# Optimization experiments

Hardware: AMD Instinct MI355X
Metric: run time of the kernel (lower is better)

Reference implementation:

```python
import jax, jax.numpy as jnp
import numpy as np

DIM = 256
NUM_HEADS = 8
REGIONS = [4, 4, 8, 8, 16, 16, 32, 32]  # per-head local window sizes
B, H_IMG, W_IMG = 8, 64, 64


def setup_inputs() -> dict:
    key = jax.random.key(0)
    ks = jax.random.split(key, 6)
    C = DIM
    s = 0.02
    return {
        'x': jax.random.normal(ks[0], (B, H_IMG * W_IMG, C), jnp.float32),
        'Wq': jax.random.normal(ks[1], (C, C), jnp.float32) * s,
        'Wkv': jax.random.normal(ks[2], (C, 2 * C), jnp.float32) * s,
        'Wlkv': jax.random.normal(ks[3], (C, 2 * C), jnp.float32) * s,
        'Wproj': jax.random.normal(ks[4], (C, C), jnp.float32) * s,
        'bproj': jnp.zeros((C,), jnp.float32),
        'H': H_IMG,
        'W': W_IMG,
    }


def _attn(q, k, v, scale):
    # softmax(q k^T * scale) v, batched over leading dims
    a = jax.nn.softmax(jnp.einsum('...qd,...kd->...qk', q, k) * scale, axis=-1)
    return jnp.einsum('...qk,...kd->...qd', a, v)


def reference(x, Wq, Wkv, Wlkv, Wproj, bproj, H, W):
    Bn, N, C = x.shape
    nh = NUM_HEADS
    Ch = C // nh
    scale = Ch ** -0.5
    M = max(REGIONS)

    q = (x @ Wq).reshape(Bn, N, nh, Ch).transpose(0, 2, 1, 3)            # [B,nh,N,Ch]
    kv = (x @ Wkv).reshape(Bn, N, 2, nh, Ch).transpose(2, 0, 3, 1, 4)    # [2,B,nh,N,Ch]
    k, v = kv[0], kv[1]

    head_outs, global_q = [], []
    for i, p in enumerate(REGIONS):
        def patch(a, p=p):  # [B,N,Ch] -> [B,NP,p*p,Ch]
            a = a.reshape(Bn, H // p, p, W // p, p, Ch)
            return a.transpose(0, 1, 3, 2, 4, 5).reshape(Bn, -1, p * p, Ch)
        qp, kp, vp = patch(q[:, i]), patch(k[:, i]), patch(v[:, i])
        # global query: mean over patches -> [B,p,p,Ch], bilinear upsample to [M,M]
        qg = qp.mean(axis=1).reshape(Bn, p, p, Ch)
        if M // p > 1:
            qg = jax.image.resize(qg, (Bn, M, M, Ch), method='bilinear')
        global_q.append(qg.reshape(Bn, M * M, Ch))
        out = _attn(qp, kp, vp, scale)                                    # [B,NP,p*p,Ch]
        head_outs.append(out.reshape(Bn, N, Ch))  # flatten in PATCH order (matches torch code)

    attn_fused = jnp.stack(head_outs, axis=1).transpose(0, 2, 1, 3).reshape(Bn, N, C)
    Q_g = jnp.stack(global_q, axis=1).transpose(0, 2, 1, 3).reshape(Bn, M * M, C)

    # blend: adaptive avg-pool attn_fused to [M,M] (exact pooling since M|H), cross-attend, upsample
    kh, kw = H // M, W // M
    pooled = attn_fused.reshape(Bn, M, kh, M, kw, C).mean(axis=(2, 4)).reshape(Bn, M * M, C)
    kv2 = (pooled @ Wlkv).reshape(Bn, M * M, 2, nh, Ch).transpose(2, 0, 3, 1, 4)
    k2, v2 = kv2[0], kv2[1]
    Qr = Q_g.reshape(Bn, M * M, nh, Ch).transpose(0, 2, 1, 3)             # [B,nh,M^2,Ch]
    gl = _attn(Qr, k2, v2, scale)                                          # [B,nh,M^2,Ch]
    gl = gl.transpose(0, 2, 1, 3).reshape(Bn, M, M, C)
    gl = jax.image.resize(gl, (Bn, H, W, C), method='bilinear').reshape(Bn, N, C)

    return (attn_fused + gl) @ Wproj + bproj
```

## Files before the change

### kernel.cpp

```cpp
#include <hip/hip_runtime.h>
#include <math.h>


typedef __attribute__((ext_vector_type(8))) short bf16x8;
typedef __attribute__((ext_vector_type(4))) short bf16x4;
typedef __attribute__((ext_vector_type(4))) float f32x4;

__device__ inline float bf2f(unsigned short u) {
  union { unsigned int i; float f; } v; v.i = ((unsigned int)u) << 16; return v.f;
}
__device__ inline unsigned short f2bf(float x) {
  union { float f; unsigned int i; } v; v.f = x;
  return (unsigned short)((v.i + 0x7FFFu + ((v.i >> 16) & 1u)) >> 16);
}
__device__ inline unsigned cvtpk(float lo, float hi) {
  unsigned r;
  asm("v_cvt_pk_bf16_f32 %0, %1, %2" : "=v"(r) : "v"(lo), "v"(hi));
  return r;
}

#define CEXP_SCALE 0.25503485947f

__global__ __launch_bounds__(256) void msa_xcast_r17(
    const float* __restrict__ x, unsigned short* __restrict__ xb)
{
  const size_t i = ((size_t)blockIdx.x * 256 + threadIdx.x) * 8;
  const float4 v0 = *reinterpret_cast<const float4*>(&x[i]);
  const float4 v1 = *reinterpret_cast<const float4*>(&x[i + 4]);
  bf16x8 o;
  o[0] = (short)f2bf(v0.x); o[1] = (short)f2bf(v0.y);
  o[2] = (short)f2bf(v0.z); o[3] = (short)f2bf(v0.w);
  o[4] = (short)f2bf(v1.x); o[5] = (short)f2bf(v1.y);
  o[6] = (short)f2bf(v1.z); o[7] = (short)f2bf(v1.w);
  *reinterpret_cast<bf16x8*>(&xb[i]) = o;
}

__global__ __launch_bounds__(256) void msa_wcast_r17(
    const float* __restrict__ Wq, const float* __restrict__ Wkv,
    const float* __restrict__ Wlkv, const float* __restrict__ Wproj,
    unsigned short* __restrict__ Wqkvt, unsigned short* __restrict__ Wlkvt,
    unsigned short* __restrict__ Wprjt)
{
  const int id = blockIdx.x * 256 + threadIdx.x;
  if (id < 196608) {
    const int r = id >> 8, k = id & 255;
    const float v = (r < 256) ? Wq[(size_t)k * 256 + r] : Wkv[(size_t)k * 512 + (r - 256)];
    Wqkvt[id] = f2bf(v);
  } else if (id < 327680) {
    const int j = id - 196608;
    const int n = j >> 8, k = j & 255;
    Wlkvt[j] = f2bf(Wlkv[(size_t)k * 512 + n]);
  } else if (id < 393216) {
    const int j = id - 327680;
    const int n = j >> 8, k = j & 255;
    Wprjt[j] = f2bf(Wproj[(size_t)k * 256 + n]);
  }
}

__global__ __launch_bounds__(256) void msa_gemm_mfma_r17(
    const unsigned short* __restrict__ Ab, const unsigned short* __restrict__ Wt,
    const float* __restrict__ bias, float* __restrict__ Cf,
    unsigned short* __restrict__ Cb, int K, int N, int qcols)
{
  __shared__ __align__(16) unsigned short A_lds[128][40];
  __shared__ __align__(16) unsigned short B_lds[128][40];

  const int tid = threadIdx.x;
  const int wave = tid >> 6, lane = tid & 63;
  const int l15 = lane & 15, g = lane >> 4;

  const int gx = gridDim.x;
  const int nwg = gx * gridDim.y;
  const int lin = blockIdx.y * gx + blockIdx.x;
  const int qq = nwg >> 3;
  const int virt = (lin & 7) * qq + (lin >> 3);
  const int by = virt / gx, bx = virt - by * gx;
  const int bm = by * 128, bn = bx * 128;

  const int wr = (wave >> 1) * 64, wc = (wave & 1) * 64;

  f32x4 acc[4][4] = {};

  for (int k0 = 0; k0 < K; k0 += 32) {
    __syncthreads();
#pragma unroll
    for (int s = 0; s < 2; ++s) {
      const int id = tid + s * 256;
      const int row = id >> 2, sg = (id & 3) << 3;
      *reinterpret_cast<bf16x8*>(&A_lds[row][sg]) =
          *reinterpret_cast<const bf16x8*>(&Ab[(size_t)(bm + row) * K + k0 + sg]);
      *reinterpret_cast<bf16x8*>(&B_lds[row][sg]) =
          *reinterpret_cast<const bf16x8*>(&Wt[(size_t)(bn + row) * K + k0 + sg]);
    }
    __syncthreads();

    bf16x8 a_frag[4], b_frag[4];
#pragma unroll
    for (int mi = 0; mi < 4; ++mi)
      a_frag[mi] = *reinterpret_cast<const bf16x8*>(&A_lds[wr + mi * 16 + l15][g << 3]);
#pragma unroll
    for (int ni = 0; ni < 4; ++ni)
      b_frag[ni] = *reinterpret_cast<const bf16x8*>(&B_lds[wc + ni * 16 + l15][g << 3]);
#pragma unroll
    for (int mi = 0; mi < 4; ++mi)
#pragma unroll
      for (int ni = 0; ni < 4; ++ni)
        acc[mi][ni] = __builtin_amdgcn_mfma_f32_16x16x32_bf16(
            a_frag[mi], b_frag[ni], acc[mi][ni], 0, 0, 0);
  }

#pragma unroll
  for (int mi = 0; mi < 4; ++mi)
#pragma unroll
    for (int ni = 0; ni < 4; ++ni) {
      const int col = bn + wc + ni * 16 + l15;
      const float cs = (col < qcols) ? CEXP_SCALE : 1.0f;
#pragma unroll
      for (int i = 0; i < 4; ++i) {
        const int row = bm + wr + mi * 16 + g * 4 + i;
        float v = acc[mi][ni][i];
        if (bias) v += bias[col];
        v *= cs;
        const size_t idx = (size_t)row * N + col;
        if (Cb) Cb[idx] = f2bf(v); else Cf[idx] = v;
      }
    }
}

__device__ inline void tile_step_r17(
    const bf16x8 k0, const bf16x8 k1, const bf16x8 v0, const bf16x8 v1,
    const bf16x8 ones, const bf16x8 qf, f32x4& o0, f32x4& o1, f32x4& o2)
{
  const f32x4 zc = {0.f, 0.f, 0.f, 0.f};
  const f32x4 st0 = __builtin_amdgcn_mfma_f32_16x16x32_bf16(k0, qf, zc, 0, 0, 0);
  const f32x4 st1 = __builtin_amdgcn_mfma_f32_16x16x32_bf16(k1, qf, zc, 0, 0, 0);
  const float e00 = exp2f(st0[0]);
  const float e01 = exp2f(st0[1]);
  const float e02 = exp2f(st0[2]);
  const float e03 = exp2f(st0[3]);
  const float e10 = exp2f(st1[0]);
  const float e11 = exp2f(st1[1]);
  const float e12 = exp2f(st1[2]);
  const float e13 = exp2f(st1[3]);
  const unsigned u0 = cvtpk(e00, e01);
  const unsigned u1 = cvtpk(e02, e03);
  const unsigned u2 = cvtpk(e10, e11);
  const unsigned u3 = cvtpk(e12, e13);
  uint4 pu = make_uint4(u0, u1, u2, u3);
  const bf16x8 pb = *reinterpret_cast<const bf16x8*>(&pu);
  o2 = __builtin_amdgcn_mfma_f32_16x16x32_bf16(ones, pb, o2, 0, 0, 0);
  o0 = __builtin_amdgcn_mfma_f32_16x16x32_bf16(v0, pb, o0, 0, 0, 0);
  o1 = __builtin_amdgcn_mfma_f32_16x16x32_bf16(v1, pb, o1, 0, 0, 0);
}

__global__ __launch_bounds__(256) void msa_attn_local_r17(
    const unsigned short* __restrict__ xqkv, unsigned short* __restrict__ attnb)
{
  __shared__ __align__(16) unsigned short K_lds[64][40];
  __shared__ __align__(16) unsigned short V_lds[32][68];

  const int fx = blockIdx.x;
  const int b = blockIdx.y;
  const int tid = threadIdx.x;

  bf16x8 ones;
#pragma unroll
  for (int i = 0; i < 8; ++i) ones[i] = (short)0x3F80;

  if (fx < 32) {
    const int head = fx >> 4;
    const int nq = (fx & 15) * 256 + tid;
    const int patch = nq >> 4;
    const int t = nq & 15;
    const int hb = patch >> 4, wb = patch & 15;
    const int n = (hb * 4 + (t >> 2)) * 64 + (wb * 4 + (t & 3));

    float qr[32];
    {
      const bf16x8* q8 = reinterpret_cast<const bf16x8*>(
          xqkv + ((size_t)b * 4096 + n) * 768 + head * 32);
#pragma unroll
      for (int i = 0; i < 4; ++i) {
        const bf16x8 v = q8[i];
#pragma unroll
        for (int j = 0; j < 8; ++j) qr[i * 8 + j] = bf2f((unsigned short)v[j]);
      }
    }
    float l = 0.f;
    float acc[32] = {};
    const int kbase = (hb * 4) * 64 + wb * 4;
    for (int kk = 0; kk < 16; ++kk) {
      const int nk = kbase + (kk >> 2) * 64 + (kk & 3);
      const unsigned short* rowp = xqkv + ((size_t)b * 4096 + nk) * 768 + head * 32;
      const bf16x8* k8p = reinterpret_cast<const bf16x8*>(rowp + 256);
      const bf16x8* v8p = reinterpret_cast<const bf16x8*>(rowp + 512);
      float s = 0.f;
#pragma unroll
      for (int i = 0; i < 4; ++i) {
        const bf16x8 k8 = k8p[i];
#pragma unroll
        for (int j = 0; j < 8; ++j) s = fmaf(qr[i * 8 + j], bf2f((unsigned short)k8[j]), s);
      }
      const float p = exp2f(s);
      l += p;
#pragma unroll
      for (int i = 0; i < 4; ++i) {
        const bf16x8 v8 = v8p[i];
#pragma unroll
        for (int j = 0; j < 8; ++j)
          acc[i * 8 + j] = fmaf(p, bf2f((unsigned short)v8[j]), acc[i * 8 + j]);
      }
    }
    const float inv = 1.f / l;
    unsigned short* dst = attnb + ((size_t)b * 4096 + nq) * 256 + head * 32;
#pragma unroll
    for (int c = 0; c < 32; ++c) dst[c] = f2bf(acc[c] * inv);
    return;
  }

  const int wave = tid >> 6, lane = tid & 63;
  const int q16 = lane & 15, h = lane >> 4;
  const int skey = tid >> 2;
  const int sh = tid & 3;

  if (fx < 160) {
    const int j = fx - 32;
    const int head = 2 + (j >> 6);
    const int patch = j & 63;
    const int hb = patch >> 3, wb = patch & 7;
    const int base = (hb * 8) * 64 + wb * 8;
    const int nq = patch * 64 + wave * 16 + q16;
    const int t = nq & 63;
    const int n = base + ((t >> 3) << 6) + (t & 7);

    const bf16x8 qfrag = *reinterpret_cast<const bf16x8*>(
        xqkv + ((size_t)b * 4096 + n) * 768 + head * 32 + 8 * h);

    f32x4 o0 = {0.f,0.f,0.f,0.f}, o1 = {0.f,0.f,0.f,0.f}, o2 = {0.f,0.f,0.f,0.f};
    {
      const int nk = base + ((skey >> 3) << 6) + (skey & 7);
      const unsigned short* row = xqkv + ((size_t)b * 4096 + nk) * 768 + head * 32;
      *reinterpret_cast<bf16x8*>(&K_lds[skey][8 * sh]) =
          *reinterpret_cast<const bf16x8*>(row + 256 + 8 * sh);
      const bf16x8 v = *reinterpret_cast<const bf16x8*>(row + 512 + 8 * sh);
#pragma unroll
      for (int jj = 0; jj < 8; ++jj)
        V_lds[8 * sh + jj][skey] = (unsigned short)v[jj];
    }
    __syncthreads();

#pragma unroll
    for (int sub = 0; sub < 2; ++sub) {
      const int s32 = sub * 32;
      const bf16x8 k0 = *reinterpret_cast<const bf16x8*>(&K_lds[s32 + q16][8 * h]);
      const bf16x8 k1 = *reinterpret_cast<const bf16x8*>(&K_lds[s32 + 16 + q16][8 * h]);
      const bf16x4 va0 = *reinterpret_cast<const bf16x4*>(&V_lds[q16][s32 + 4 * h]);
      const bf16x4 vb0 = *reinterpret_cast<const bf16x4*>(&V_lds[q16][s32 + 16 + 4 * h]);
      const bf16x4 va1 = *reinterpret_cast<const bf16x4*>(&V_lds[16 + q16][s32 + 4 * h]);
      const bf16x4 vb1 = *reinterpret_cast<const bf16x4*>(&V_lds[16 + q16][s32 + 16 + 4 * h]);
      bf16x8 v0, v1;
#pragma unroll
      for (int i = 0; i < 4; ++i) {
        v0[i] = va0[i]; v0[4 + i] = vb0[i];
        v1[i] = va1[i]; v1[4 + i] = vb1[i];
      }
      tile_step_r17(k0, k1, v0, v1, ones, qfrag, o0, o1, o2);
    }

    const float inv = 1.f / o2[0];
    unsigned short* dst = attnb + ((size_t)b * 4096 + nq) * 256 + head * 32;
    uint2 w0, w1;
    w0.x = (unsigned)f2bf(o0[0] * inv) | ((unsigned)f2bf(o0[1] * inv) << 16);
    w0.y = (unsigned)f2bf(o0[2] * inv) | ((unsigned)f2bf(o0[3] * inv) << 16);
    w1.x = (unsigned)f2bf(o1[0] * inv) | ((unsigned)f2bf(o1[1] * inv) << 16);
    w1.y = (unsigned)f2bf(o1[2] * inv) | ((unsigned)f2bf(o1[3] * inv) << 16);
    *reinterpret_cast<uint2*>(dst + 4 * h) = w0;
    *reinterpret_cast<uint2*>(dst + 16 + 4 * h) = w1;
    return;
  }

  {
    const int j = fx - 160;
    const int head = 4 + (j >> 4);
    const int xb = j & 15;
    const int lp = (head < 6) ? 4 : 5;
    const int p = 1 << lp;
    const int pm1 = p - 1;
    const int P2 = p * p;
    const int patch = (xb * 256) >> (2 * lp);
    const int nbp = 64 >> lp;
    const int hb = patch / nbp, wb = patch - (patch / nbp) * nbp;
    const int base = ((hb << lp)) * 64 + (wb << lp);

    const int q0 = xb * 256 + wave * 64;
    const int nqA = q0 + q16, nqB = q0 + 16 + q16, nqC = q0 + 32 + q16, nqD = q0 + 48 + q16;

    bf16x8 qfA, qfB, qfC, qfD;
    {
      int tt = nqA & (P2 - 1);
      qfA = *reinterpret_cast<const bf16x8*>(
          xqkv + ((size_t)b * 4096 + base + ((tt >> lp) << 6) + (tt & pm1)) * 768 + head * 32 + 8 * h);
      tt = nqB & (P2 - 1);
      qfB = *reinterpret_cast<const bf16x8*>(
          xqkv + ((size_t)b * 4096 + base + ((tt >> lp) << 6) + (tt & pm1)) * 768 + head * 32 + 8 * h);
      tt = nqC & (P2 - 1);
      qfC = *reinterpret_cast<const bf16x8*>(
          xqkv + ((size_t)b * 4096 + base + ((tt >> lp) << 6) + (tt & pm1)) * 768 + head * 32 + 8 * h);
      tt = nqD & (P2 - 1);
      qfD = *reinterpret_cast<const bf16x8*>(
          xqkv + ((size_t)b * 4096 + base + ((tt >> lp) << 6) + (tt & pm1)) * 768 + head * 32 + 8 * h);
    }

    f32x4 o0A = {0.f,0.f,0.f,0.f}, o1A = {0.f,0.f,0.f,0.f}, o2A = {0.f,0.f,0.f,0.f};
    f32x4 o0B = {0.f,0.f,0.f,0.f}, o1B = {0.f,0.f,0.f,0.f}, o2B = {0.f,0.f,0.f,0.f};
    f32x4 o0C = {0.f,0.f,0.f,0.f}, o1C = {0.f,0.f,0.f,0.f}, o2C = {0.f,0.f,0.f,0.f};
    f32x4 o0D = {0.f,0.f,0.f,0.f}, o1D = {0.f,0.f,0.f,0.f}, o2D = {0.f,0.f,0.f,0.f};

    {
      const int nk0 = base + ((skey >> lp) << 6) + (skey & pm1);
      const unsigned short* row = xqkv + ((size_t)b * 4096 + nk0) * 768 + head * 32;
      const bf16x8 kr = *reinterpret_cast<const bf16x8*>(row + 256 + 8 * sh);
      const bf16x8 vr = *reinterpret_cast<const bf16x8*>(row + 512 + 8 * sh);
      *reinterpret_cast<bf16x8*>(&K_lds[skey][8 * sh]) = kr;
#pragma unroll
      for (int jj = 0; jj < 8; ++jj)
        V_lds[8 * sh + jj][skey] = (unsigned short)vr[jj];
    }
    __syncthreads();

    for (int kc = 0; kc < P2; kc += 64) {
      const bool more = (kc + 64) < P2;
      bf16x8 krn = {}, vrn = {};
      if (more) {
        const int kk = kc + 64 + skey;
        const int nk = base + ((kk >> lp) << 6) + (kk & pm1);
        const unsigned short* row = xqkv + ((size_t)b * 4096 + nk) * 768 + head * 32;
        krn = *reinterpret_cast<const bf16x8*>(row + 256 + 8 * sh);
        vrn = *reinterpret_cast<const bf16x8*>(row + 512 + 8 * sh);
      }

#pragma unroll
      for (int sub = 0; sub < 2; ++sub) {
        const int s32 = sub * 32;
        const bf16x8 k0 = *reinterpret_cast<const bf16x8*>(&K_lds[s32 + q16][8 * h]);
        const bf16x8 k1 = *reinterpret_cast<const bf16x8*>(&K_lds[s32 + 16 + q16][8 * h]);
        const bf16x4 va0 = *reinterpret_cast<const bf16x4*>(&V_lds[q16][s32 + 4 * h]);
        const bf16x4 vb0 = *reinterpret_cast<const bf16x4*>(&V_lds[q16][s32 + 16 + 4 * h]);
        const bf16x4 va1 = *reinterpret_cast<const bf16x4*>(&V_lds[16 + q16][s32 + 4 * h]);
        const bf16x4 vb1 = *reinterpret_cast<const bf16x4*>(&V_lds[16 + q16][s32 + 16 + 4 * h]);
        bf16x8 v0, v1;
#pragma unroll
        for (int i = 0; i < 4; ++i) {
          v0[i] = va0[i]; v0[4 + i] = vb0[i];
          v1[i] = va1[i]; v1[4 + i] = vb1[i];
        }
        tile_step_r17(k0, k1, v0, v1, ones, qfA, o0A, o1A, o2A);
        tile_step_r17(k0, k1, v0, v1, ones, qfB, o0B, o1B, o2B);
        tile_step_r17(k0, k1, v0, v1, ones, qfC, o0C, o1C, o2C);
        tile_step_r17(k0, k1, v0, v1, ones, qfD, o0D, o1D, o2D);
      }
      __syncthreads();
      if (more) {
        *reinterpret_cast<bf16x8*>(&K_lds[skey][8 * sh]) = krn;
#pragma unroll
        for (int jj = 0; jj < 8; ++jj)
          V_lds[8 * sh + jj][skey] = (unsigned short)vrn[jj];
      }
      __syncthreads();
    }

#define R17L_EPI(O0, O1, O2, NQ)                                               \
    {                                                                          \
      const float inv = 1.f / O2[0];                                           \
      unsigned short* dst = attnb + ((size_t)b * 4096 + (NQ)) * 256 + head * 32;\
      uint2 w0, w1;                                                            \
      w0.x = (unsigned)f2bf(O0[0] * inv) | ((unsigned)f2bf(O0[1] * inv) << 16);\
      w0.y = (unsigned)f2bf(O0[2] * inv) | ((unsigned)f2bf(O0[3] * inv) << 16);\
      w1.x = (unsigned)f2bf(O1[0] * inv) | ((unsigned)f2bf(O1[1] * inv) << 16);\
      w1.y = (unsigned)f2bf(O1[2] * inv) | ((unsigned)f2bf(O1[3] * inv) << 16);\
      *reinterpret_cast<uint2*>(dst + 4 * h) = w0;                             \
      *reinterpret_cast<uint2*>(dst + 16 + 4 * h) = w1;                        \
    }
    R17L_EPI(o0A, o1A, o2A, nqA)
    R17L_EPI(o0B, o1B, o2B, nqB)
    R17L_EPI(o0C, o1C, o2C, nqC)
    R17L_EPI(o0D, o1D, o2D, nqD)
#undef R17L_EPI
  }
}

__global__ __launch_bounds__(256) void msa_attn_glob_r17(
    const unsigned short* __restrict__ Qg, const unsigned short* __restrict__ kv2,
    float* __restrict__ gl)
{
  __shared__ __align__(16) unsigned short K_lds[64][40];
  __shared__ __align__(16) unsigned short V_lds[32][68];

  const int tid = threadIdx.x;
  const int wave = tid >> 6, lane = tid & 63;
  const int q16 = lane & 15, h = lane >> 4;
  const int b = blockIdx.y;
  const int head = blockIdx.z;

  bf16x8 ones;
#pragma unroll
  for (int i = 0; i < 8; ++i) ones[i] = (short)0x3F80;

  const int q0 = blockIdx.x * 256 + wave * 64;
  const int nqA = q0 + q16, nqB = q0 + 16 + q16, nqC = q0 + 32 + q16, nqD = q0 + 48 + q16;

  const bf16x8 qfA = *reinterpret_cast<const bf16x8*>(
      Qg + ((size_t)b * 1024 + nqA) * 256 + head * 32 + 8 * h);
  const bf16x8 qfB = *reinterpret_cast<const bf16x8*>(
      Qg + ((size_t)b * 1024 + nqB) * 256 + head * 32 + 8 * h);
  const bf16x8 qfC = *reinterpret_cast<const bf16x8*>(
      Qg + ((size_t)b * 1024 + nqC) * 256 + head * 32 + 8 * h);
  const bf16x8 qfD = *reinterpret_cast<const bf16x8*>(
      Qg + ((size_t)b * 1024 + nqD) * 256 + head * 32 + 8 * h);

  f32x4 o0A = {0.f,0.f,0.f,0.f}, o1A = {0.f,0.f,0.f,0.f}, o2A = {0.f,0.f,0.f,0.f};
  f32x4 o0B = {0.f,0.f,0.f,0.f}, o1B = {0.f,0.f,0.f,0.f}, o2B = {0.f,0.f,0.f,0.f};
  f32x4 o0C = {0.f,0.f,0.f,0.f}, o1C = {0.f,0.f,0.f,0.f}, o2C = {0.f,0.f,0.f,0.f};
  f32x4 o0D = {0.f,0.f,0.f,0.f}, o1D = {0.f,0.f,0.f,0.f}, o2D = {0.f,0.f,0.f,0.f};

  const int skey = tid >> 2;
  const int sh = tid & 3;

  {
    const unsigned short* row = kv2 + ((size_t)b * 1024 + skey) * 512 + head * 32;
    const bf16x8 kr = *reinterpret_cast<const bf16x8*>(row + 8 * sh);
    const bf16x8 vr = *reinterpret_cast<const bf16x8*>(row + 256 + 8 * sh);
    *reinterpret_cast<bf16x8*>(&K_lds[skey][8 * sh]) = kr;
#pragma unroll
    for (int jj = 0; jj < 8; ++jj)
      V_lds[8 * sh + jj][skey] = (unsigned short)vr[jj];
  }
  __syncthreads();

  for (int kc = 0; kc < 1024; kc += 64) {
    const bool more = (kc + 64) < 1024;
    bf16x8 krn = {}, vrn = {};
    if (more) {
      const unsigned short* row = kv2 + ((size_t)b * 1024 + kc + 64 + skey) * 512 + head * 32;
      krn = *reinterpret_cast<const bf16x8*>(row + 8 * sh);
      vrn = *reinterpret_cast<const bf16x8*>(row + 256 + 8 * sh);
    }

#pragma unroll
    for (int sub = 0; sub < 2; ++sub) {
      const int s32 = sub * 32;
      const bf16x8 k0 = *reinterpret_cast<const bf16x8*>(&K_lds[s32 + q16][8 * h]);
      const bf16x8 k1 = *reinterpret_cast<const bf16x8*>(&K_lds[s32 + 16 + q16][8 * h]);
      const bf16x4 va0 = *reinterpret_cast<const bf16x4*>(&V_lds[q16][s32 + 4 * h]);
      const bf16x4 vb0 = *reinterpret_cast<const bf16x4*>(&V_lds[q16][s32 + 16 + 4 * h]);
      const bf16x4 va1 = *reinterpret_cast<const bf16x4*>(&V_lds[16 + q16][s32 + 4 * h]);
      const bf16x4 vb1 = *reinterpret_cast<const bf16x4*>(&V_lds[16 + q16][s32 + 16 + 4 * h]);
      bf16x8 v0, v1;
#pragma unroll
      for (int i = 0; i < 4; ++i) {
        v0[i] = va0[i]; v0[4 + i] = vb0[i];
        v1[i] = va1[i]; v1[4 + i] = vb1[i];
      }
      tile_step_r17(k0, k1, v0, v1, ones, qfA, o0A, o1A, o2A);
      tile_step_r17(k0, k1, v0, v1, ones, qfB, o0B, o1B, o2B);
      tile_step_r17(k0, k1, v0, v1, ones, qfC, o0C, o1C, o2C);
      tile_step_r17(k0, k1, v0, v1, ones, qfD, o0D, o1D, o2D);
    }
    __syncthreads();
    if (more) {
      *reinterpret_cast<bf16x8*>(&K_lds[skey][8 * sh]) = krn;
#pragma unroll
      for (int jj = 0; jj < 8; ++jj)
        V_lds[8 * sh + jj][skey] = (unsigned short)vrn[jj];
    }
    __syncthreads();
  }

#define R17G_EPI(O0, O1, O2, NQ)                                               \
  {                                                                            \
    const float inv = 1.f / O2[0];                                             \
    float* dst = gl + ((size_t)b * 1024 + (NQ)) * 256 + head * 32;             \
    float4 w0, w1;                                                             \
    w0.x = O0[0] * inv; w0.y = O0[1] * inv;                                    \
    w0.z = O0[2] * inv; w0.w = O0[3] * inv;                                    \
    w1.x = O1[0] * inv; w1.y = O1[1] * inv;                                    \
    w1.z = O1[2] * inv; w1.w = O1[3] * inv;                                    \
    *reinterpret_cast<float4*>(dst + 4 * h) = w0;                              \
    *reinterpret_cast<float4*>(dst + 16 + 4 * h) = w1;                         \
  }
  R17G_EPI(o0A, o1A, o2A, nqA)
  R17G_EPI(o0B, o1B, o2B, nqB)
  R17G_EPI(o0C, o1C, o2C, nqC)
  R17G_EPI(o0D, o1D, o2D, nqD)
#undef R17G_EPI
}

__global__ __launch_bounds__(256) void msa_qg_reduce_r17(
    const unsigned short* __restrict__ xqkv, float* __restrict__ qg_all)
{
  __shared__ float red[256];
  const int head = blockIdx.z;
  const int lp = (head < 2) ? 2 : (head < 4) ? 3 : (head < 6) ? 4 : 5;
  const int p = 1 << lp;
  const int P2 = p * p;
  const int nbp = 64 >> lp;
  const int npat = nbp * nbp;
  const int R = (lp <= 3) ? 8 : 1;
  const int total = P2 * 32 * R;
  const int gid = blockIdx.x * 256 + threadIdx.x;
  if (gid >= total) return;
  const int b = blockIdx.y;

  const int c = gid & 31;
  const int tr = gid >> 5;
  const int r = tr & (R - 1);
  const int t = tr >> ((R == 8) ? 3 : 0);
  const int hp = t >> lp, wp = t & (p - 1);

  const unsigned short* src = xqkv + (size_t)b * 4096 * 768 + head * 32 + c;
  float s = 0.f;
  for (int j = r; j < npat; j += R) {
    const int hb = j / nbp, wb = j - (j / nbp) * nbp;
    const int n = ((hb << lp) + hp) * 64 + (wb << lp) + wp;
    s += bf2f(src[(size_t)n * 768]);
  }

  if (R == 8) {
    red[threadIdx.x] = s;
    __syncthreads();
    if (r < 4) red[threadIdx.x] += red[threadIdx.x + 128];
    __syncthreads();
    if (r < 2) red[threadIdx.x] += red[threadIdx.x + 64];
    __syncthreads();
    if (r == 0) {
      s = red[threadIdx.x] + red[threadIdx.x + 32];
      qg_all[((size_t)b * 8 + head) * 32768 + (size_t)t * 32 + c] = s / (float)npat;
    }
  } else {
    qg_all[((size_t)b * 8 + head) * 32768 + (size_t)t * 32 + c] = s / (float)npat;
  }
}

__global__ __launch_bounds__(256) void msa_qg_upsample_r17(
    const float* __restrict__ qg_all, unsigned short* __restrict__ Qg)
{
  const int head = blockIdx.z;
  const int p = (head < 2) ? 4 : (head < 4) ? 8 : (head < 6) ? 16 : 32;
  const int e = blockIdx.x * 256 + threadIdx.x;
  const int b = blockIdx.y;
  const int mlin = e >> 5, c = e & 31;
  const int mi = mlin >> 5, mj = mlin & 31;
  const float* src = qg_all + ((size_t)b * 8 + head) * 32768;
  float v;
  if (p == 32) {
    v = src[(size_t)mlin * 32 + c];
  } else {
    const float s = (float)p / 32.0f;
    const float xf = (mj + 0.5f) * s - 0.5f;
    const float yf = (mi + 0.5f) * s - 0.5f;
    const float xfl = floorf(xf), yfl = floorf(yf);
    const float fx = xf - xfl, fy = yf - yfl;
    const int x0 = (int)xfl, y0 = (int)yfl;
    const int x0c = max(0, min(p - 1, x0)), x1c = max(0, min(p - 1, x0 + 1));
    const int y0c = max(0, min(p - 1, y0)), y1c = max(0, min(p - 1, y0 + 1));
    const float v00 = src[(size_t)(y0c * p + x0c) * 32 + c];
    const float v01 = src[(size_t)(y0c * p + x1c) * 32 + c];
    const float v10 = src[(size_t)(y1c * p + x0c) * 32 + c];
    const float v11 = src[(size_t)(y1c * p + x1c) * 32 + c];
    v = (1.f - fy) * ((1.f - fx) * v00 + fx * v01)
      + fy * ((1.f - fx) * v10 + fx * v11);
  }
  Qg[((size_t)b * 1024 + mlin) * 256 + head * 32 + c] = f2bf(v);
}

__global__ __launch_bounds__(256) void msa_pool_r17(
    const unsigned short* __restrict__ attn, unsigned short* __restrict__ pooled)
{
  const int c = threadIdx.x;
  const int mlin = blockIdx.x;
  const int b = blockIdx.y;
  const int mi = mlin >> 5, mj = mlin & 31;
  const size_t base = (size_t)b * 4096;
  const int r0 = mi * 2, q0 = mj * 2;
  float s = bf2f(attn[(base + (r0 * 64 + q0)) * 256 + c])
          + bf2f(attn[(base + (r0 * 64 + q0 + 1)) * 256 + c])
          + bf2f(attn[(base + ((r0 + 1) * 64 + q0)) * 256 + c])
          + bf2f(attn[(base + ((r0 + 1) * 64 + q0 + 1)) * 256 + c]);
  pooled[((size_t)b * 1024 + mlin) * 256 + c] = f2bf(s * 0.25f);
}

__global__ __launch_bounds__(256) void msa_blend_r17(
    const float* __restrict__ gl, unsigned short* __restrict__ attn)
{
  const int c = threadIdx.x;
  const int n = blockIdx.x;
  const int b = blockIdx.y;
  const int hh = n >> 6, w = n & 63;
  const float xf = (w + 0.5f) * 0.5f - 0.5f;
  const float yf = (hh + 0.5f) * 0.5f - 0.5f;
  const float xfl = floorf(xf), yfl = floorf(yf);
  const float fx = xf - xfl, fy = yf - yfl;
  const int x0 = (int)xfl, y0 = (int)yfl;
  const int x0c = max(0, min(31, x0)), x1c = max(0, min(31, x0 + 1));
  const int y0c = max(0, min(31, y0)), y1c = max(0, min(31, y0 + 1));
  const float* g = gl + (size_t)b * 1024 * 256;
  const float v00 = g[(size_t)(y0c * 32 + x0c) * 256 + c];
  const float v01 = g[(size_t)(y0c * 32 + x1c) * 256 + c];
  const float v10 = g[(size_t)(y1c * 32 + x0c) * 256 + c];
  const float v11 = g[(size_t)(y1c * 32 + x1c) * 256 + c];
  const float v = (1.f - fy) * ((1.f - fx) * v00 + fx * v01)
                + fy * ((1.f - fx) * v10 + fx * v11);
  const size_t idx = ((size_t)b * 4096 + n) * 256 + c;
  attn[idx] = f2bf(bf2f(attn[idx]) + v);
}

extern "C" void kernel_launch(void* const* d_in, const int* in_sizes, int n_in,
                              void* d_out, int out_size, void* d_ws, size_t ws_size,
                              hipStream_t stream)
{
  const float* x     = (const float*)d_in[0];
  const float* Wq    = (const float*)d_in[1];
  const float* Wkv   = (const float*)d_in[2];
  const float* Wlkv  = (const float*)d_in[3];
  const float* Wproj = (const float*)d_in[4];
  const float* bproj = (const float*)d_in[5];

  char* ws = (char*)d_ws;
  unsigned short* xqkv  = (unsigned short*)(ws + 0);
  unsigned short* attnb = (unsigned short*)(ws + 50331648ull);
  unsigned short* Qg    = (unsigned short*)(ws + 67108864ull);
  float* qg_all = (float*)(ws + 71303168ull);
  unsigned short* Wqkvt = (unsigned short*)(ws + 79691776ull);
  unsigned short* Wlkvt = (unsigned short*)(ws + 80084992ull);
  unsigned short* Wprjt = (unsigned short*)(ws + 80347136ull);
  float* gl     = (float*)(ws + 80478208ull);
  unsigned short* xb    = (unsigned short*)(ws + 88866816ull);
  unsigned short* pooled = (unsigned short*)(ws + 0);
  unsigned short* kv2    = (unsigned short*)(ws + 16777216ull);

  msa_xcast_r17<<<dim3(4096), 256, 0, stream>>>(x, xb);
  msa_wcast_r17<<<dim3(1536), 256, 0, stream>>>(Wq, Wkv, Wlkv, Wproj, Wqkvt, Wlkvt, Wprjt);

  msa_gemm_mfma_r17<<<dim3(6, 256), 256, 0, stream>>>(xb, Wqkvt, nullptr, nullptr, xqkv, 256, 768, 256);

  msa_qg_reduce_r17<<<dim3(128, 8, 8), 256, 0, stream>>>(xqkv, qg_all);
  msa_qg_upsample_r17<<<dim3(128, 8, 8), 256, 0, stream>>>(qg_all, Qg);

  msa_attn_local_r17<<<dim3(224, 8), 256, 0, stream>>>(xqkv, attnb);

  msa_pool_r17<<<dim3(1024, 8), 256, 0, stream>>>(attnb, pooled);
  msa_gemm_mfma_r17<<<dim3(4, 64), 256, 0, stream>>>(pooled, Wlkvt, nullptr, nullptr, kv2, 256, 512, 0);

  msa_attn_glob_r17<<<dim3(4, 8, 8), 256, 0, stream>>>(Qg, kv2, gl);

  msa_blend_r17<<<dim3(4096, 8), 256, 0, stream>>>(gl, attnb);
  msa_gemm_mfma_r17<<<dim3(2, 256), 256, 0, stream>>>(attnb, Wprjt, bproj, (float*)d_out, nullptr, 256, 256, 0);

  (void)in_sizes; (void)n_in; (void)out_size; (void)ws_size;
}
```

Measured before the change: 218.6 us.

## Split long attention key ranges across two workgroups with combine kernels

```diff
diff --git a/kernel.cpp b/kernel.cpp
--- a/kernel.cpp
+++ b/kernel.cpp
@@ -21,7 +21,7 @@
 
 #define CEXP_SCALE 0.25503485947f
 
-__global__ __launch_bounds__(256) void msa_xcast_r17(
+__global__ __launch_bounds__(256) void msa_xcast_r18(
     const float* __restrict__ x, unsigned short* __restrict__ xb)
 {
   const size_t i = ((size_t)blockIdx.x * 256 + threadIdx.x) * 8;
@@ -35,7 +35,7 @@
   *reinterpret_cast<bf16x8*>(&xb[i]) = o;
 }
 
-__global__ __launch_bounds__(256) void msa_wcast_r17(
+__global__ __launch_bounds__(256) void msa_wcast_r18(
     const float* __restrict__ Wq, const float* __restrict__ Wkv,
     const float* __restrict__ Wlkv, const float* __restrict__ Wproj,
     unsigned short* __restrict__ Wqkvt, unsigned short* __restrict__ Wlkvt,
@@ -57,7 +57,7 @@
   }
 }
 
-__global__ __launch_bounds__(256) void msa_gemm_mfma_r17(
+__global__ __launch_bounds__(256) void msa_gemm_mfma_r18(
     const unsigned short* __restrict__ Ab, const unsigned short* __restrict__ Wt,
     const float* __restrict__ bias, float* __restrict__ Cf,
     unsigned short* __restrict__ Cb, int K, int N, int qcols)
@@ -127,7 +127,7 @@
     }
 }
 
-__device__ inline void tile_step_r17(
+__device__ inline void tile_step_r18(
     const bf16x8 k0, const bf16x8 k1, const bf16x8 v0, const bf16x8 v1,
     const bf16x8 ones, const bf16x8 qf, f32x4& o0, f32x4& o1, f32x4& o2)
 {
@@ -153,8 +153,9 @@
   o1 = __builtin_amdgcn_mfma_f32_16x16x32_bf16(v1, pb, o1, 0, 0, 0);
 }
 
-__global__ __launch_bounds__(256) void msa_attn_local_r17(
-    const unsigned short* __restrict__ xqkv, unsigned short* __restrict__ attnb)
+__global__ __launch_bounds__(256) void msa_attn_local_r18(
+    const unsigned short* __restrict__ xqkv, unsigned short* __restrict__ attnb,
+    float* __restrict__ po, float* __restrict__ pl)
 {
   __shared__ __align__(16) unsigned short K_lds[64][40];
   __shared__ __align__(16) unsigned short V_lds[32][68];
@@ -264,7 +265,7 @@
         v0[i] = va0[i]; v0[4 + i] = vb0[i];
         v1[i] = va1[i]; v1[4 + i] = vb1[i];
       }
-      tile_step_r17(k0, k1, v0, v1, ones, qfrag, o0, o1, o2);
+      tile_step_r18(k0, k1, v0, v1, ones, qfrag, o0, o1, o2);
     }
 
     const float inv = 1.f / o2[0];
@@ -279,97 +280,106 @@
     return;
   }
 
+  int head, lp, xb2, split, kstart, kend;
+  if (fx < 192) {
+    const int j = fx - 160;
+    head = 4 + (j >> 4); xb2 = j & 15; split = 0; lp = 4;
+    kstart = 0; kend = 256;
+  } else {
+    const int j = fx - 192;
+    head = 6 + (j >> 5);
+    const int r = j & 31;
+    xb2 = r >> 1; split = r & 1; lp = 5;
+    kstart = split * 512; kend = kstart + 512;
+  }
+  const int p = 1 << lp;
+  const int pm1 = p - 1;
+  const int P2 = p * p;
+  const int nbp = 64 >> lp;
+  const int patch = (xb2 * 256) >> (2 * lp);
+  const int hb = patch / nbp, wb = patch - (patch / nbp) * nbp;
+  const int base = ((hb << lp)) * 64 + (wb << lp);
+
+  const int q0 = xb2 * 256 + wave * 64;
+  const int nqA = q0 + q16, nqB = q0 + 16 + q16, nqC = q0 + 32 + q16, nqD = q0 + 48 + q16;
+
+  bf16x8 qfA, qfB, qfC, qfD;
   {
-    const int j = fx - 160;
-    const int head = 4 + (j >> 4);
-    const int xb = j & 15;
-    const int lp = (head < 6) ? 4 : 5;
-    const int p = 1 << lp;
-    const int pm1 = p - 1;
-    const int P2 = p * p;
-    const int patch = (xb * 256) >> (2 * lp);
-    const int nbp = 64 >> lp;
-    const int hb = patch / nbp, wb = patch - (patch / nbp) * nbp;
-    const int base = ((hb << lp)) * 64 + (wb << lp);
-
-    const int q0 = xb * 256 + wave * 64;
-    const int nqA = q0 + q16, nqB = q0 + 16 + q16, nqC = q0 + 32 + q16, nqD = q0 + 48 + q16;
-
-    bf16x8 qfA, qfB, qfC, qfD;
-    {
-      int tt = nqA & (P2 - 1);
-      qfA = *reinterpret_cast<const bf16x8*>(
-          xqkv + ((size_t)b * 4096 + base + ((tt >> lp) << 6) + (tt & pm1)) * 768 + head * 32 + 8 * h);
-      tt = nqB & (P2 - 1);
-      qfB = *reinterpret_cast<const bf16x8*>(
-          xqkv + ((size_t)b * 4096 + base + ((tt >> lp) << 6) + (tt & pm1)) * 768 + head * 32 + 8 * h);
-      tt = nqC & (P2 - 1);
-      qfC = *reinterpret_cast<const bf16x8*>(
-          xqkv + ((size_t)b * 4096 + base + ((tt >> lp) << 6) + (tt & pm1)) * 768 + head * 32 + 8 * h);
-      tt = nqD & (P2 - 1);
-      qfD = *reinterpret_cast<const bf16x8*>(
-          xqkv + ((size_t)b * 4096 + base + ((tt >> lp) << 6) + (tt & pm1)) * 768 + head * 32 + 8 * h);
-    }
-
-    f32x4 o0A = {0.f,0.f,0.f,0.f}, o1A = {0.f,0.f,0.f,0.f}, o2A = {0.f,0.f,0.f,0.f};
-    f32x4 o0B = {0.f,0.f,0.f,0.f}, o1B = {0.f,0.f,0.f,0.f}, o2B = {0.f,0.f,0.f,0.f};
-    f32x4 o0C = {0.f,0.f,0.f,0.f}, o1C = {0.f,0.f,0.f,0.f}, o2C = {0.f,0.f,0.f,0.f};
-    f32x4 o0D = {0.f,0.f,0.f,0.f}, o1D = {0.f,0.f,0.f,0.f}, o2D = {0.f,0.f,0.f,0.f};
-
-    {
-      const int nk0 = base + ((skey >> lp) << 6) + (skey & pm1);
-      const unsigned short* row = xqkv + ((size_t)b * 4096 + nk0) * 768 + head * 32;
-      const bf16x8 kr = *reinterpret_cast<const bf16x8*>(row + 256 + 8 * sh);
-      const bf16x8 vr = *reinterpret_cast<const bf16x8*>(row + 512 + 8 * sh);
-      *reinterpret_cast<bf16x8*>(&K_lds[skey][8 * sh]) = kr;
+    int tt = nqA & (P2 - 1);
+    qfA = *reinterpret_cast<const bf16x8*>(
+        xqkv + ((size_t)b * 4096 + base + ((tt >> lp) << 6) + (tt & pm1)) * 768 + head * 32 + 8 * h);
+    tt = nqB & (P2 - 1);
+    qfB = *reinterpret_cast<const bf16x8*>(
+        xqkv + ((size_t)b * 4096 + base + ((tt >> lp) << 6) + (tt & pm1)) * 768 + head * 32 + 8 * h);
+    tt = nqC & (P2 - 1);
+    qfC = *reinterpret_cast<const bf16x8*>(
+        xqkv + ((size_t)b * 4096 + base + ((tt >> lp) << 6) + (tt & pm1)) * 768 + head * 32 + 8 * h);
+    tt = nqD & (P2 - 1);
+    qfD = *reinterpret_cast<const bf16x8*>(
+        xqkv + ((size_t)b * 4096 + base + ((tt >> lp) << 6) + (tt & pm1)) * 768 + head * 32 + 8 * h);
+  }
+
+  f32x4 o0A = {0.f,0.f,0.f,0.f}, o1A = {0.f,0.f,0.f,0.f}, o2A = {0.f,0.f,0.f,0.f};
+  f32x4 o0B = {0.f,0.f,0.f,0.f}, o1B = {0.f,0.f,0.f,0.f}, o2B = {0.f,0.f,0.f,0.f};
+  f32x4 o0C = {0.f,0.f,0.f,0.f}, o1C = {0.f,0.f,0.f,0.f}, o2C = {0.f,0.f,0.f,0.f};
+  f32x4 o0D = {0.f,0.f,0.f,0.f}, o1D = {0.f,0.f,0.f,0.f}, o2D = {0.f,0.f,0.f,0.f};
+
+  {
+    const int kk = kstart + skey;
+    const int nk0 = base + ((kk >> lp) << 6) + (kk & pm1);
+    const unsigned short* row = xqkv + ((size_t)b * 4096 + nk0) * 768 + head * 32;
+    const bf16x8 kr = *reinterpret_cast<const bf16x8*>(row + 256 + 8 * sh);
+    const bf16x8 vr = *reinterpret_cast<const bf16x8*>(row + 512 + 8 * sh);
+    *reinterpret_cast<bf16x8*>(&K_lds[skey][8 * sh]) = kr;
+#pragma unroll
+    for (int jj = 0; jj < 8; ++jj)
+      V_lds[8 * sh + jj][skey] = (unsigned short)vr[jj];
+  }
+  __syncthreads();
+
+  for (int kc = kstart; kc < kend; kc += 64) {
+    const bool more = (kc + 64) < kend;
+    bf16x8 krn = {}, vrn = {};
+    if (more) {
+      const int kk = kc + 64 + skey;
+      const int nk = base + ((kk >> lp) << 6) + (kk & pm1);
+      const unsigned short* row = xqkv + ((size_t)b * 4096 + nk) * 768 + head * 32;
+      krn = *reinterpret_cast<const bf16x8*>(row + 256 + 8 * sh);
+      vrn = *reinterpret_cast<const bf16x8*>(row + 512 + 8 * sh);
+    }
+
+#pragma unroll
+    for (int sub = 0; sub < 2; ++sub) {
+      const int s32 = sub * 32;
+      const bf16x8 k0 = *reinterpret_cast<const bf16x8*>(&K_lds[s32 + q16][8 * h]);
+      const bf16x8 k1 = *reinterpret_cast<const bf16x8*>(&K_lds[s32 + 16 + q16][8 * h]);
+      const bf16x4 va0 = *reinterpret_cast<const bf16x4*>(&V_lds[q16][s32 + 4 * h]);
+      const bf16x4 vb0 = *reinterpret_cast<const bf16x4*>(&V_lds[q16][s32 + 16 + 4 * h]);
+      const bf16x4 va1 = *reinterpret_cast<const bf16x4*>(&V_lds[16 + q16][s32 + 4 * h]);
+      const bf16x4 vb1 = *reinterpret_cast<const bf16x4*>(&V_lds[16 + q16][s32 + 16 + 4 * h]);
+      bf16x8 v0, v1;
+#pragma unroll
+      for (int i = 0; i < 4; ++i) {
+        v0[i] = va0[i]; v0[4 + i] = vb0[i];
+        v1[i] = va1[i]; v1[4 + i] = vb1[i];
+      }
+      tile_step_r18(k0, k1, v0, v1, ones, qfA, o0A, o1A, o2A);
+      tile_step_r18(k0, k1, v0, v1, ones, qfB, o0B, o1B, o2B);
+      tile_step_r18(k0, k1, v0, v1, ones, qfC, o0C, o1C, o2C);
+      tile_step_r18(k0, k1, v0, v1, ones, qfD, o0D, o1D, o2D);
+    }
+    __syncthreads();
+    if (more) {
+      *reinterpret_cast<bf16x8*>(&K_lds[skey][8 * sh]) = krn;
 #pragma unroll
       for (int jj = 0; jj < 8; ++jj)
-        V_lds[8 * sh + jj][skey] = (unsigned short)vr[jj];
-    }
-    __syncthreads();
-
-    for (int kc = 0; kc < P2; kc += 64) {
-      const bool more = (kc + 64) < P2;
-      bf16x8 krn = {}, vrn = {};
-      if (more) {
-        const int kk = kc + 64 + skey;
-        const int nk = base + ((kk >> lp) << 6) + (kk & pm1);
-        const unsigned short* row = xqkv + ((size_t)b * 4096 + nk) * 768 + head * 32;
-        krn = *reinterpret_cast<const bf16x8*>(row + 256 + 8 * sh);
-        vrn = *reinterpret_cast<const bf16x8*>(row + 512 + 8 * sh);
-      }
-
-#pragma unroll
-      for (int sub = 0; sub < 2; ++sub) {
-        const int s32 = sub * 32;
-        const bf16x8 k0 = *reinterpret_cast<const bf16x8*>(&K_lds[s32 + q16][8 * h]);
-        const bf16x8 k1 = *reinterpret_cast<const bf16x8*>(&K_lds[s32 + 16 + q16][8 * h]);
-        const bf16x4 va0 = *reinterpret_cast<const bf16x4*>(&V_lds[q16][s32 + 4 * h]);
-        const bf16x4 vb0 = *reinterpret_cast<const bf16x4*>(&V_lds[q16][s32 + 16 + 4 * h]);
-        const bf16x4 va1 = *reinterpret_cast<const bf16x4*>(&V_lds[16 + q16][s32 + 4 * h]);
-        const bf16x4 vb1 = *reinterpret_cast<const bf16x4*>(&V_lds[16 + q16][s32 + 16 + 4 * h]);
-        bf16x8 v0, v1;
-#pragma unroll
-        for (int i = 0; i < 4; ++i) {
-          v0[i] = va0[i]; v0[4 + i] = vb0[i];
-          v1[i] = va1[i]; v1[4 + i] = vb1[i];
-        }
-        tile_step_r17(k0, k1, v0, v1, ones, qfA, o0A, o1A, o2A);
-        tile_step_r17(k0, k1, v0, v1, ones, qfB, o0B, o1B, o2B);
-        tile_step_r17(k0, k1, v0, v1, ones, qfC, o0C, o1C, o2C);
-        tile_step_r17(k0, k1, v0, v1, ones, qfD, o0D, o1D, o2D);
-      }
-      __syncthreads();
-      if (more) {
-        *reinterpret_cast<bf16x8*>(&K_lds[skey][8 * sh]) = krn;
-#pragma unroll
-        for (int jj = 0; jj < 8; ++jj)
-          V_lds[8 * sh + jj][skey] = (unsigned short)vrn[jj];
-      }
-      __syncthreads();
-    }
-
-#define R17L_EPI(O0, O1, O2, NQ)                                               \
+        V_lds[8 * sh + jj][skey] = (unsigned short)vrn[jj];
+    }
+    __syncthreads();
+  }
+
+  if (lp == 4) {
+#define R18L_EPI(O0, O1, O2, NQ)                                               \
     {                                                                          \
       const float inv = 1.f / O2[0];                                           \
       unsigned short* dst = attnb + ((size_t)b * 4096 + (NQ)) * 256 + head * 32;\
@@ -381,17 +391,51 @@
       *reinterpret_cast<uint2*>(dst + 4 * h) = w0;                             \
       *reinterpret_cast<uint2*>(dst + 16 + 4 * h) = w1;                        \
     }
-    R17L_EPI(o0A, o1A, o2A, nqA)
-    R17L_EPI(o0B, o1B, o2B, nqB)
-    R17L_EPI(o0C, o1C, o2C, nqC)
-    R17L_EPI(o0D, o1D, o2D, nqD)
-#undef R17L_EPI
-  }
-}
-
-__global__ __launch_bounds__(256) void msa_attn_glob_r17(
+    R18L_EPI(o0A, o1A, o2A, nqA)
+    R18L_EPI(o0B, o1B, o2B, nqB)
+    R18L_EPI(o0C, o1C, o2C, nqC)
+    R18L_EPI(o0D, o1D, o2D, nqD)
+#undef R18L_EPI
+  } else {
+    const int head2 = head - 6;
+    const size_t pb0 = ((((size_t)split * 2 + head2) * 8 + b) * 4096);
+#define R18P_EPI(O0, O1, O2, NQ)                                               \
+    {                                                                          \
+      float* dst = po + (pb0 + (NQ)) * 32;                                     \
+      float4 w0, w1;                                                           \
+      w0.x = O0[0]; w0.y = O0[1]; w0.z = O0[2]; w0.w = O0[3];                  \
+      w1.x = O1[0]; w1.y = O1[1]; w1.z = O1[2]; w1.w = O1[3];                  \
+      *reinterpret_cast<float4*>(dst + 4 * h) = w0;                            \
+      *reinterpret_cast<float4*>(dst + 16 + 4 * h) = w1;                       \
+      if (h == 0) pl[pb0 + (NQ)] = O2[0];                                      \
+    }
+    R18P_EPI(o0A, o1A, o2A, nqA)
+    R18P_EPI(o0B, o1B, o2B, nqB)
+    R18P_EPI(o0C, o1C, o2C, nqC)
+    R18P_EPI(o0D, o1D, o2D, nqD)
+#undef R18P_EPI
+  }
+}
+
+__global__ __launch_bounds__(256) void msa_p32comb_r18(
+    const float* __restrict__ po, const float* __restrict__ pl,
+    unsigned short* __restrict__ attnb)
+{
+  const int e = blockIdx.x * 256 + threadIdx.x;
+  const int b = blockIdx.y;
+  const int head2 = e >> 17;
+  const int rem = e & 131071;
+  const int nq = rem >> 5, c = rem & 31;
+  const size_t i0 = ((((size_t)0 * 2 + head2) * 8 + b) * 4096 + nq);
+  const size_t i1 = ((((size_t)1 * 2 + head2) * 8 + b) * 4096 + nq);
+  const float o = po[i0 * 32 + c] + po[i1 * 32 + c];
+  const float l = pl[i0] + pl[i1];
+  attnb[((size_t)b * 4096 + nq) * 256 + (6 + head2) * 32 + c] = f2bf(o / l);
+}
+
+__global__ __launch_bounds__(256) void msa_attn_glob_r18(
     const unsigned short* __restrict__ Qg, const unsigned short* __restrict__ kv2,
-    float* __restrict__ gl)
+    float* __restrict__ go, float* __restrict__ gll)
 {
   __shared__ __align__(16) unsigned short K_lds[64][40];
   __shared__ __align__(16) unsigned short V_lds[32][68];
@@ -401,12 +445,15 @@
   const int q16 = lane & 15, h = lane >> 4;
   const int b = blockIdx.y;
   const int head = blockIdx.z;
+  const int xb2 = blockIdx.x >> 1;
+  const int split = blockIdx.x & 1;
+  const int kstart = split * 512, kend = kstart + 512;
 
   bf16x8 ones;
 #pragma unroll
   for (int i = 0; i < 8; ++i) ones[i] = (short)0x3F80;
 
-  const int q0 = blockIdx.x * 256 + wave * 64;
+  const int q0 = xb2 * 256 + wave * 64;
   const int nqA = q0 + q16, nqB = q0 + 16 + q16, nqC = q0 + 32 + q16, nqD = q0 + 48 + q16;
 
   const bf16x8 qfA = *reinterpret_cast<const bf16x8*>(
@@ -427,7 +474,7 @@
   const int sh = tid & 3;
 
   {
-    const unsigned short* row = kv2 + ((size_t)b * 1024 + skey) * 512 + head * 32;
+    const unsigned short* row = kv2 + ((size_t)b * 1024 + kstart + skey) * 512 + head * 32;
     const bf16x8 kr = *reinterpret_cast<const bf16x8*>(row + 8 * sh);
     const bf16x8 vr = *reinterpret_cast<const bf16x8*>(row + 256 + 8 * sh);
     *reinterpret_cast<bf16x8*>(&K_lds[skey][8 * sh]) = kr;
@@ -437,8 +484,8 @@
   }
   __syncthreads();
 
-  for (int kc = 0; kc < 1024; kc += 64) {
-    const bool more = (kc + 64) < 1024;
+  for (int kc = kstart; kc < kend; kc += 64) {
+    const bool more = (kc + 64) < kend;
     bf16x8 krn = {}, vrn = {};
     if (more) {
       const unsigned short* row = kv2 + ((size_t)b * 1024 + kc + 64 + skey) * 512 + head * 32;
@@ -461,10 +508,10 @@
         v0[i] = va0[i]; v0[4 + i] = vb0[i];
         v1[i] = va1[i]; v1[4 + i] = vb1[i];
       }
-      tile_step_r17(k0, k1, v0, v1, ones, qfA, o0A, o1A, o2A);
-      tile_step_r17(k0, k1, v0, v1, ones, qfB, o0B, o1B, o2B);
-      tile_step_r17(k0, k1, v0, v1, ones, qfC, o0C, o1C, o2C);
-      tile_step_r17(k0, k1, v0, v1, ones, qfD, o0D, o1D, o2D);
+      tile_step_r18(k0, k1, v0, v1, ones, qfA, o0A, o1A, o2A);
+      tile_step_r18(k0, k1, v0, v1, ones, qfB, o0B, o1B, o2B);
+      tile_step_r18(k0, k1, v0, v1, ones, qfC, o0C, o1C, o2C);
+      tile_step_r18(k0, k1, v0, v1, ones, qfD, o0D, o1D, o2D);
     }
     __syncthreads();
     if (more) {
@@ -476,26 +523,41 @@
     __syncthreads();
   }
 
-#define R17G_EPI(O0, O1, O2, NQ)                                               \
+  const size_t gb0 = ((((size_t)split * 8 + b) * 8 + head) * 1024);
+#define R18G_EPI(O0, O1, O2, NQ)                                               \
   {                                                                            \
-    const float inv = 1.f / O2[0];                                             \
-    float* dst = gl + ((size_t)b * 1024 + (NQ)) * 256 + head * 32;             \
+    float* dst = go + (gb0 + (NQ)) * 32;                                       \
     float4 w0, w1;                                                             \
-    w0.x = O0[0] * inv; w0.y = O0[1] * inv;                                    \
-    w0.z = O0[2] * inv; w0.w = O0[3] * inv;                                    \
-    w1.x = O1[0] * inv; w1.y = O1[1] * inv;                                    \
-    w1.z = O1[2] * inv; w1.w = O1[3] * inv;                                    \
+    w0.x = O0[0]; w0.y = O0[1]; w0.z = O0[2]; w0.w = O0[3];                    \
+    w1.x = O1[0]; w1.y = O1[1]; w1.z = O1[2]; w1.w = O1[3];                    \
     *reinterpret_cast<float4*>(dst + 4 * h) = w0;                              \
     *reinterpret_cast<float4*>(dst + 16 + 4 * h) = w1;                         \
-  }
-  R17G_EPI(o0A, o1A, o2A, nqA)
-  R17G_EPI(o0B, o1B, o2B, nqB)
-  R17G_EPI(o0C, o1C, o2C, nqC)
-  R17G_EPI(o0D, o1D, o2D, nqD)
-#undef R17G_EPI
-}
-
-__global__ __launch_bounds__(256) void msa_qg_reduce_r17(
+    if (h == 0) gll[gb0 + (NQ)] = O2[0];                                       \
+  }
+  R18G_EPI(o0A, o1A, o2A, nqA)
+  R18G_EPI(o0B, o1B, o2B, nqB)
+  R18G_EPI(o0C, o1C, o2C, nqC)
+  R18G_EPI(o0D, o1D, o2D, nqD)
+#undef R18G_EPI
+}
+
+__global__ __launch_bounds__(256) void msa_globcomb_r18(
+    const float* __restrict__ go, const float* __restrict__ gll,
+    float* __restrict__ gl)
+{
+  const int e = blockIdx.x * 256 + threadIdx.x;
+  const int b = blockIdx.y;
+  const int head = e >> 15;
+  const int rem = e & 32767;
+  const int nq = rem >> 5, c = rem & 31;
+  const size_t i0 = ((((size_t)0 * 8 + b) * 8 + head) * 1024 + nq);
+  const size_t i1 = ((((size_t)1 * 8 + b) * 8 + head) * 1024 + nq);
+  const float o = go[i0 * 32 + c] + go[i1 * 32 + c];
+  const float l = gll[i0] + gll[i1];
+  gl[((size_t)b * 1024 + nq) * 256 + head * 32 + c] = o / l;
+}
+
+__global__ __launch_bounds__(256) void msa_qg_reduce_r18(
     const unsigned short* __restrict__ xqkv, float* __restrict__ qg_all)
 {
   __shared__ float red[256];
@@ -541,7 +603,7 @@
   }
 }
 
-__global__ __launch_bounds__(256) void msa_qg_upsample_r17(
+__global__ __launch_bounds__(256) void msa_qg_upsample_r18(
     const float* __restrict__ qg_all, unsigned short* __restrict__ Qg)
 {
   const int head = blockIdx.z;
@@ -573,7 +635,7 @@
   Qg[((size_t)b * 1024 + mlin) * 256 + head * 32 + c] = f2bf(v);
 }
 
-__global__ __launch_bounds__(256) void msa_pool_r17(
+__global__ __launch_bounds__(256) void msa_pool_r18(
     const unsigned short* __restrict__ attn, unsigned short* __restrict__ pooled)
 {
   const int c = threadIdx.x;
@@ -589,7 +651,7 @@
   pooled[((size_t)b * 1024 + mlin) * 256 + c] = f2bf(s * 0.25f);
 }
 
-__global__ __launch_bounds__(256) void msa_blend_r17(
+__global__ __launch_bounds__(256) void msa_blend_r18(
     const float* __restrict__ gl, unsigned short* __restrict__ attn)
 {
   const int c = threadIdx.x;
@@ -635,26 +697,32 @@
   unsigned short* Wprjt = (unsigned short*)(ws + 80347136ull);
   float* gl     = (float*)(ws + 80478208ull);
   unsigned short* xb    = (unsigned short*)(ws + 88866816ull);
+  float* po  = (float*)(ws + 105644032ull);
+  float* pl  = (float*)(ws + 122421248ull);
+  float* go  = (float*)(ws + 123469824ull);
+  float* gll = (float*)(ws + 140247040ull);
   unsigned short* pooled = (unsigned short*)(ws + 0);
   unsigned short* kv2    = (unsigned short*)(ws + 16777216ull);
 
-  msa_xcast_r17<<<dim3(4096), 256, 0, stream>>>(x, xb);
-  msa_wcast_r17<<<dim3(1536), 256, 0, stream>>>(Wq, Wkv, Wlkv, Wproj, Wqkvt, Wlkvt, Wprjt);
-
-  msa_gemm_mfma_r17<<<dim3(6, 256), 256, 0, stream>>>(xb, Wqkvt, nullptr, nullptr, xqkv, 256, 768, 256);
-
-  msa_qg_reduce_r17<<<dim3(128, 8, 8), 256, 0, stream>>>(xqkv, qg_all);
-  msa_qg_upsample_r17<<<dim3(128, 8, 8), 256, 0, stream>>>(qg_all, Qg);
-
-  msa_attn_local_r17<<<dim3(224, 8), 256, 0, stream>>>(xqkv, attnb);
-
-  msa_pool_r17<<<dim3(1024, 8), 256, 0, stream>>>(attnb, pooled);
-  msa_gemm_mfma_r17<<<dim3(4, 64), 256, 0, stream>>>(pooled, Wlkvt, nullptr, nullptr, kv2, 256, 512, 0);
-
-  msa_attn_glob_r17<<<dim3(4, 8, 8), 256, 0, stream>>>(Qg, kv2, gl);
-
-  msa_blend_r17<<<dim3(4096, 8), 256, 0, stream>>>(gl, attnb);
-  msa_gemm_mfma_r17<<<dim3(2, 256), 256, 0, stream>>>(attnb, Wprjt, bproj, (float*)d_out, nullptr, 256, 256, 0);
+  msa_xcast_r18<<<dim3(4096), 256, 0, stream>>>(x, xb);
+  msa_wcast_r18<<<dim3(1536), 256, 0, stream>>>(Wq, Wkv, Wlkv, Wproj, Wqkvt, Wlkvt, Wprjt);
+
+  msa_gemm_mfma_r18<<<dim3(6, 256), 256, 0, stream>>>(xb, Wqkvt, nullptr, nullptr, xqkv, 256, 768, 256);
+
+  msa_qg_reduce_r18<<<dim3(128, 8, 8), 256, 0, stream>>>(xqkv, qg_all);
+  msa_qg_upsample_r18<<<dim3(128, 8, 8), 256, 0, stream>>>(qg_all, Qg);
+
+  msa_attn_local_r18<<<dim3(256, 8), 256, 0, stream>>>(xqkv, attnb, po, pl);
+  msa_p32comb_r18<<<dim3(1024, 8), 256, 0, stream>>>(po, pl, attnb);
+
+  msa_pool_r18<<<dim3(1024, 8), 256, 0, stream>>>(attnb, pooled);
+  msa_gemm_mfma_r18<<<dim3(4, 64), 256, 0, stream>>>(pooled, Wlkvt, nullptr, nullptr, kv2, 256, 512, 0);
+
+  msa_attn_glob_r18<<<dim3(8, 8, 8), 256, 0, stream>>>(Qg, kv2, go, gll);
+  msa_globcomb_r18<<<dim3(1024, 8), 256, 0, stream>>>(go, gll, gl);
+
+  msa_blend_r18<<<dim3(4096, 8), 256, 0, stream>>>(gl, attnb);
+  msa_gemm_mfma_r18<<<dim3(2, 256), 256, 0, stream>>>(attnb, Wprjt, bproj, (float*)d_out, nullptr, 256, 256, 0);
 
   (void)in_sizes; (void)n_in; (void)out_size; (void)ws_size;
 }
```

New measurement: 211.2 us. 3.4% less time.
